# Optimization experiments

Hardware: AMD Instinct MI355X
Metric: run time of the kernel (lower is better)

The kernel has to match this reference:

```python
import jax, jax.numpy as jnp
import numpy as np

H = W = 32
C = 384
NH = 12
HEAD = C // NH
SCALE = HEAD ** -0.5
WS = 8            # window size
SS = 4            # shift size
N = WS * WS       # tokens per window (64)
NW = (H // WS) * (W // WS)  # windows per image (16)
HIDDEN = 4 * C
EPS = 1e-5
SQRT_2_OVER_PI = float(np.sqrt(2.0 / np.pi))


def _relative_position_index():
    ch = np.arange(WS)
    coords = np.stack(np.meshgrid(ch, ch, indexing='ij')).reshape(2, -1)  # [2, N]
    rel = (coords[:, :, None] - coords[:, None, :]).transpose(1, 2, 0)    # [N, N, 2]
    rel[:, :, 0] += WS - 1
    rel[:, :, 1] += WS - 1
    rel[:, :, 0] *= 2 * WS - 1
    return rel.sum(-1)  # [N, N] int


def _attn_mask():
    img = np.zeros((H, W), np.float32)
    sl = (slice(0, -WS), slice(-WS, -SS), slice(-SS, None))
    cnt = 0
    for hs in sl:
        for ws_ in sl:
            img[hs, ws_] = cnt
            cnt += 1
    m = img.reshape(H // WS, WS, W // WS, WS).transpose(0, 2, 1, 3).reshape(-1, N)  # [nW, N]
    am = m[:, None, :] - m[:, :, None]
    return np.where(am != 0, -100.0, 0.0).astype(np.float32)  # [nW, N, N]


REL_IDX = jnp.asarray(_relative_position_index())
ATTN_MASK = jnp.asarray(_attn_mask())


def _gelu(x):
    return x * 0.5 * (1.0 + jnp.tanh(SQRT_2_OVER_PI * (x + 0.044715 * x ** 3)))


def _layernorm(x, g, b):
    mu = jnp.mean(x, axis=-1, keepdims=True)
    var = jnp.mean(jnp.square(x - mu), axis=-1, keepdims=True)
    return (x - mu) * jax.lax.rsqrt(var + EPS) * g + b


def _window_partition(x):  # [B,H,W,C] -> [B*nW, N, C]
    B = x.shape[0]
    x = x.reshape(B, H // WS, WS, W // WS, WS, C).transpose(0, 1, 3, 2, 4, 5)
    return x.reshape(-1, N, C)


def _window_reverse(w, B):  # [B*nW, N, C] -> [B,H,W,C]
    x = w.reshape(B, H // WS, W // WS, WS, WS, C).transpose(0, 1, 3, 2, 4, 5)
    return x.reshape(B, H, W, C)


def setup_inputs() -> dict:
    key = jax.random.key(0)
    ks = jax.random.split(key, 16)
    s = 0.02
    return {
        'x': jax.random.normal(ks[0], (32, H * W, C), jnp.float32),
        'norm1_g': jnp.ones((C,), jnp.float32),
        'norm1_b': jnp.zeros((C,), jnp.float32),
        'qkv_w': jax.random.normal(ks[1], (C, 3 * C), jnp.float32) * s,
        'qkv_b': jnp.zeros((3 * C,), jnp.float32),
        'rel_bias_table': jax.random.normal(ks[2], ((2 * WS - 1) ** 2, NH), jnp.float32) * s,
        'proj_w': jax.random.normal(ks[3], (C, C), jnp.float32) * s,
        'proj_b': jnp.zeros((C,), jnp.float32),
        'norm2_g': jnp.ones((C,), jnp.float32),
        'norm2_b': jnp.zeros((C,), jnp.float32),
        'fc1_w': jax.random.normal(ks[4], (C, HIDDEN), jnp.float32) * s,
        'fc1_b': jnp.zeros((HIDDEN,), jnp.float32),
        'fc2_w': jax.random.normal(ks[5], (HIDDEN, C), jnp.float32) * s,
        'fc2_b': jnp.zeros((C,), jnp.float32),
    }


def reference(x, norm1_g, norm1_b, qkv_w, qkv_b, rel_bias_table, proj_w, proj_b,
              norm2_g, norm2_b, fc1_w, fc1_b, fc2_w, fc2_b):
    B = x.shape[0]
    shortcut = x
    y = _layernorm(x, norm1_g, norm1_b).reshape(B, H, W, C)
    y = jnp.roll(y, shift=(-SS, -SS), axis=(1, 2))          # cyclic shift
    win = _window_partition(y)                               # [B*nW, N, C]

    qkv = (win @ qkv_w + qkv_b).reshape(-1, N, 3, NH, HEAD).transpose(2, 0, 3, 1, 4)
    q, k, v = qkv[0], qkv[1], qkv[2]                         # [B*nW, NH, N, HEAD]
    attn = jnp.einsum('whnd,whmd->whnm', q * SCALE, k)       # [B*nW, NH, N, N]

    bias = rel_bias_table[REL_IDX.reshape(-1)].reshape(N, N, NH).transpose(2, 0, 1)
    attn = attn + bias[None]
    attn = attn.reshape(B, NW, NH, N, N) + ATTN_MASK[None, :, None]
    attn = jax.nn.softmax(attn.reshape(-1, NH, N, N), axis=-1)

    out = jnp.einsum('whnm,whmd->wnhd', attn, v).reshape(-1, N, C)
    out = out @ proj_w + proj_b                              # [B*nW, N, C]

    y = _window_reverse(out, B)
    y = jnp.roll(y, shift=(SS, SS), axis=(1, 2)).reshape(B, H * W, C)

    x = shortcut + y                                         # drop_path is identity (eval)
    h = _layernorm(x, norm2_g, norm2_b)
    h = _gelu(h @ fc1_w + fc1_b) @ fc2_w + fc2_b
    return x + h
```

## Files before the change

### kernel.cpp

```cpp
#include <hip/hip_runtime.h>
#include <hip/hip_bf16.h>
#include <math.h>

typedef __hip_bfloat16 bf16;
typedef __attribute__((ext_vector_type(8))) short short8;
typedef __attribute__((ext_vector_type(4))) float floatx4;

static constexpr int TOK = 32768;
static constexpr int CDIM = 384;
static constexpr int HID = 1536;

__device__ __forceinline__ bf16 f2bf(float v) { return __float2bfloat16(v); }

__device__ __forceinline__ unsigned short bf_bits(float a) {
  bf16 h = __float2bfloat16(a);
  unsigned short u;
  __builtin_memcpy(&u, &h, 2);
  return u;
}
__device__ __forceinline__ unsigned pack2(float a, float b) {
  return (unsigned)bf_bits(a) | ((unsigned)bf_bits(b) << 16);
}

typedef const __attribute__((address_space(1))) unsigned gas_t;
typedef __attribute__((address_space(3))) unsigned las_t;
__device__ __forceinline__ void gload16(const bf16* g, const bf16* l) {
  __builtin_amdgcn_global_load_lds((gas_t*)g, (las_t*)l, 16, 0, 0);
}

__global__ __launch_bounds__(256) void k_convt4(
    const float* __restrict__ s0, bf16* __restrict__ d0,
    const float* __restrict__ s1, bf16* __restrict__ d1,
    const float* __restrict__ s2, bf16* __restrict__ d2,
    const float* __restrict__ s3, bf16* __restrict__ d3) {
  int tid = blockIdx.x * 256 + threadIdx.x;
  const float* src; bf16* dst; int Kd, Nd, off;
  if (tid < 442368) { src = s0; dst = d0; Kd = 384; Nd = 1152; off = tid; }
  else if (tid < 589824) { src = s1; dst = d1; Kd = 384; Nd = 384; off = tid - 442368; }
  else if (tid < 1179648) { src = s2; dst = d2; Kd = 384; Nd = 1536; off = tid - 589824; }
  else { src = s3; dst = d3; Kd = 1536; Nd = 384; off = tid - 1179648; }
  int k = off / Nd, n = off - k * Nd;
  dst[(size_t)n * Kd + k] = f2bf(src[off]);
}

__global__ __launch_bounds__(256) void k_ln1(const float* __restrict__ x,
                                             const float* __restrict__ g,
                                             const float* __restrict__ b,
                                             bf16* __restrict__ out) {
  int wt = blockIdx.x * 4 + (threadIdx.x >> 6);
  int lane = threadIdx.x & 63;
  int win = wt >> 6, ntok = wt & 63;
  int bimg = win >> 4, wi = win & 15;
  int sh = (((wi >> 2) << 3) + (ntok >> 3) + 4) & 31;
  int sw = (((wi & 3) << 3) + (ntok & 7) + 4) & 31;
  const float* xr = x + ((size_t)bimg * 1024 + sh * 32 + sw) * CDIM;
  float v[6]; float s = 0.f, ss = 0.f;
#pragma unroll
  for (int j = 0; j < 6; ++j) {
    float t = xr[j * 64 + lane];
    v[j] = t; s += t; ss += t * t;
  }
#pragma unroll
  for (int off = 32; off > 0; off >>= 1) {
    s += __shfl_xor(s, off, 64);
    ss += __shfl_xor(ss, off, 64);
  }
  float mu = s * (1.f / 384.f);
  float var = ss * (1.f / 384.f) - mu * mu;
  float rs = rsqrtf(var + 1e-5f);
  bf16* orow = out + (size_t)wt * CDIM;
#pragma unroll
  for (int j = 0; j < 6; ++j) {
    int c = j * 64 + lane;
    orow[c] = f2bf((v[j] - mu) * rs * g[c] + b[c]);
  }
}

__global__ __launch_bounds__(256) void k_ln2(const float* __restrict__ x1,
                                             const float* __restrict__ g,
                                             const float* __restrict__ b,
                                             bf16* __restrict__ out) {
  int t = blockIdx.x * 4 + (threadIdx.x >> 6);
  int lane = threadIdx.x & 63;
  const float* xr = x1 + (size_t)t * CDIM;
  float v[6]; float s = 0.f, ss = 0.f;
#pragma unroll
  for (int j = 0; j < 6; ++j) {
    float q = xr[j * 64 + lane];
    v[j] = q; s += q; ss += q * q;
  }
#pragma unroll
  for (int off = 32; off > 0; off >>= 1) {
    s += __shfl_xor(s, off, 64);
    ss += __shfl_xor(ss, off, 64);
  }
  float mu = s * (1.f / 384.f);
  float var = ss * (1.f / 384.f) - mu * mu;
  float rs = rsqrtf(var + 1e-5f);
  bf16* orow = out + (size_t)t * CDIM;
#pragma unroll
  for (int j = 0; j < 6; ++j) {
    int c = j * 64 + lane;
    orow[c] = f2bf((v[j] - mu) * rs * g[c] + b[c]);
  }
}

template <int K, int EPI, int NT>
__global__ __launch_bounds__(256) void k_gemm(const bf16* __restrict__ A,
                                              const bf16* __restrict__ Bt,
                                              const float* __restrict__ bias,
                                              const float* __restrict__ extra,
                                              void* __restrict__ outp) {
  __shared__ __attribute__((aligned(16))) char pool[49152];
  bf16* A0 = (bf16*)pool;
  bf16* B0 = (bf16*)(pool + 8192);
  bf16* A1 = (bf16*)(pool + 16384);
  bf16* B1 = (bf16*)(pool + 24576);
  bf16* A2 = (bf16*)(pool + 32768);
  bf16* B2 = (bf16*)(pool + 40960);

  const int tid = threadIdx.x;
  const int wv = tid >> 6, lane = tid & 63;

  const int flat = blockIdx.x;
  const int xcd = flat & 7;
  const int idx = flat >> 3;
  const int rpx = (gridDim.x >> 3) / NT;
  const int cb = idx % NT;
  const int rb = idx / NT;
  const int mblk = (xcd * rpx + rb) * 128, nblk = cb * 128;

  const int srow = lane >> 3;
  const int sc = (lane & 7) ^ srow;
  const int srow2 = 2 * srow + (sc >> 2);
  const int gco = (sc & 3) * 8;
  const bf16* gaw = A + (size_t)(mblk + wv * 32 + srow2) * K + gco;
  const bf16* gbw = Bt + (size_t)(nblk + wv * 32 + srow2) * K + gco;
  bf16* lA0 = A0 + wv * 1024; bf16* lB0 = B0 + wv * 1024;
  bf16* lA1 = A1 + wv * 1024; bf16* lB1 = B1 + wv * 1024;
  bf16* lA2 = A2 + wv * 1024; bf16* lB2 = B2 + wv * 1024;

  const int wr = wv >> 1, wc = wv & 1;
  const int mr = lane & 15, q = lane >> 4;
  const int slot8 = ((((mr & 1) << 2) | q) ^ (mr >> 1)) * 8;
  const int faOff = (wr * 32 + (mr >> 1)) * 64 + slot8;
  const int fbOff = (wc * 32 + (mr >> 1)) * 64 + slot8;

  floatx4 acc[4][4];
#pragma unroll
  for (int i = 0; i < 4; ++i)
#pragma unroll
    for (int j = 0; j < 4; ++j) acc[i][j] = floatx4{0.f, 0.f, 0.f, 0.f};

#define VM4() asm volatile("s_waitcnt vmcnt(4)" ::: "memory")
#define VM0() asm volatile("s_waitcnt vmcnt(0)" ::: "memory")
#define BAR() __builtin_amdgcn_s_barrier()

#define STAGE(LA, LB, KOFF) do { \
    gload16(gaw + (KOFF), (LA)); \
    gload16(gaw + (KOFF) + 16 * K, (LA) + 512); \
    gload16(gbw + (KOFF), (LB)); \
    gload16(gbw + (KOFF) + 16 * K, (LB) + 512); \
  } while (0)

#define COMPUTE(ABASE, BBASE) do { \
    short8 a_[4], b_[4]; \
    _Pragma("unroll") \
    for (int mt = 0; mt < 4; ++mt) a_[mt] = *(const short8*)((ABASE) + faOff + mt * 512); \
    _Pragma("unroll") \
    for (int nt = 0; nt < 4; ++nt) b_[nt] = *(const short8*)((BBASE) + fbOff + nt * 512); \
    _Pragma("unroll") \
    for (int mt = 0; mt < 4; ++mt) \
      _Pragma("unroll") \
      for (int nt = 0; nt < 4; ++nt) \
        acc[mt][nt] = __builtin_amdgcn_mfma_f32_16x16x32_bf16(a_[mt], b_[nt], acc[mt][nt], 0, 0, 0); \
  } while (0)

  STAGE(lA0, lB0, 0);
  STAGE(lA1, lB1, 32);
  for (int k0 = 0; k0 < K - 96; k0 += 96) {
    VM4(); BAR(); STAGE(lA2, lB2, k0 + 64);  COMPUTE(A0, B0);
    VM4(); BAR(); STAGE(lA0, lB0, k0 + 96);  COMPUTE(A1, B1);
    VM4(); BAR(); STAGE(lA1, lB1, k0 + 128); COMPUTE(A2, B2);
  }
  VM4(); BAR(); STAGE(lA2, lB2, K - 32); COMPUTE(A0, B0);
  VM4(); BAR();                          COMPUTE(A1, B1);
  VM0(); BAR();                          COMPUTE(A2, B2);
#undef STAGE
#undef COMPUTE
#undef VM4
#undef VM0
#undef BAR

  __syncthreads();
  float* epsw = (float*)pool + wv * (16 * 68);
  const int rr = lane >> 2, c0 = (lane & 3) * 16;
#pragma unroll
  for (int mt = 0; mt < 4; ++mt) {
#pragma unroll
    for (int nt = 0; nt < 4; ++nt)
#pragma unroll
      for (int r = 0; r < 4; ++r)
        epsw[(q * 4 + r) * 68 + nt * 16 + mr] = acc[mt][nt][r];
    float v[16];
#pragma unroll
    for (int j = 0; j < 4; ++j) {
      float4 t = *(const float4*)&epsw[rr * 68 + c0 + j * 4];
      v[j * 4 + 0] = t.x; v[j * 4 + 1] = t.y; v[j * 4 + 2] = t.z; v[j * 4 + 3] = t.w;
    }
    const int grow = mblk + wr * 64 + mt * 16 + rr;
    const int gcol = nblk + wc * 64 + c0;

    if constexpr (EPI == 0) {
      int win = grow >> 6, ntok = grow & 63;
      int s = gcol / 384;
      int rem = gcol - s * 384;
      int h = rem >> 5, d0 = rem & 31;
      bf16* op = (bf16*)outp + (((size_t)s * 512 + win) * 12 + h) * 2048 + ntok * 32 + d0;
      uint4 pk;
      float bv[16];
#pragma unroll
      for (int j = 0; j < 16; ++j) bv[j] = v[j] + bias[gcol + j];
      pk.x = pack2(bv[0], bv[1]); pk.y = pack2(bv[2], bv[3]);
      pk.z = pack2(bv[4], bv[5]); pk.w = pack2(bv[6], bv[7]);
      *(uint4*)op = pk;
      pk.x = pack2(bv[8], bv[9]); pk.y = pack2(bv[10], bv[11]);
      pk.z = pack2(bv[12], bv[13]); pk.w = pack2(bv[14], bv[15]);
      *(uint4*)(op + 8) = pk;
    } else if constexpr (EPI == 1) {
      int win = grow >> 6, ntok = grow & 63;
      int bimg = win >> 4, wi = win & 15;
      int hh = (((wi >> 2) << 3) + (ntok >> 3) + 4) & 31;
      int ww = (((wi & 3) << 3) + (ntok & 7) + 4) & 31;
      size_t t = (size_t)bimg * 1024 + hh * 32 + ww;
      float* op = (float*)outp + t * CDIM + gcol;
      const float* xr = extra + t * CDIM + gcol;
#pragma unroll
      for (int j = 0; j < 4; ++j) {
        float4 xv = *(const float4*)(xr + j * 4);
        float4 ov;
        ov.x = xv.x + v[j * 4 + 0] + bias[gcol + j * 4 + 0];
        ov.y = xv.y + v[j * 4 + 1] + bias[gcol + j * 4 + 1];
        ov.z = xv.z + v[j * 4 + 2] + bias[gcol + j * 4 + 2];
        ov.w = xv.w + v[j * 4 + 3] + bias[gcol + j * 4 + 3];
        *(float4*)(op + j * 4) = ov;
      }
    }
  }
}

__global__ __launch_bounds__(512, 2) void k_mlp(const bf16* __restrict__ A,
                                                const bf16* __restrict__ W1t,
                                                const bf16* __restrict__ W2t,
                                                const float* __restrict__ b1,
                                                const float* __restrict__ b2,
                                                const float* __restrict__ x1,
                                                float* __restrict__ out) {
  __shared__ __attribute__((aligned(16))) char pool[131072];
  bf16* A0 = (bf16*)pool;
  bf16* A1 = (bf16*)(pool + 8192);
  bf16* A2 = (bf16*)(pool + 16384);
  bf16* W10 = (bf16*)(pool + 24576);
  bf16* W11 = (bf16*)(pool + 32768);
  bf16* W12 = (bf16*)(pool + 40960);
  bf16* hs = (bf16*)(pool + 49152);
  bf16* W2sA = (bf16*)(pool + 81920);
  bf16* W2sB = (bf16*)(pool + 106496);

  const int tid = threadIdx.x;
  const int wv = tid >> 6, lane = tid & 63;
  const int mblk = blockIdx.x * 128;

  const int srow = lane >> 3;
  const int sc = (lane & 7) ^ srow;
  const int srow2 = 2 * srow + (sc >> 2);
  const int gco = (sc & 3) * 8;

  const bf16* ga = A + (size_t)(mblk + wv * 16 + srow2) * 384 + gco;
  const bf16* g1 = W1t + (size_t)(wv * 16 + srow2) * 384 + gco;
  const bf16* g2 = W2t + (size_t)(wv * 48 + srow2) * 1536 + gco;

  const int wr1 = wv >> 2, wc1 = wv & 3;
  const int mr = lane & 15, q = lane >> 4;
  const int slot8 = ((((mr & 1) << 2) | q) ^ (mr >> 1)) * 8;
  const int faOff1 = (wr1 * 32 + (mr >> 1)) * 64 + slot8;
  const int fbOff1 = (wc1 * 16 + (mr >> 1)) * 64 + slot8;
  const int fbOff2 = (wc1 * 48 + (mr >> 1)) * 64 + slot8;
  const size_t hb = (size_t)(wr1 * 64 + mr) * 128;
  int px[4];
#pragma unroll
  for (int kk = 0; kk < 4; ++kk)
    px[kk] = (((kk & 2) << 2) | ((((kk & 1) << 2) | q) ^ (mr & 7))) * 8;

  floatx4 acc1[4][2];
  floatx4 acc2[4][6];
#pragma unroll
  for (int i = 0; i < 4; ++i) {
#pragma unroll
    for (int j = 0; j < 2; ++j) acc1[i][j] = floatx4{0.f, 0.f, 0.f, 0.f};
#pragma unroll
    for (int j = 0; j < 6; ++j) acc2[i][j] = floatx4{0.f, 0.f, 0.f, 0.f};
  }

#define VMW(N) asm volatile("s_waitcnt vmcnt(" #N ")" ::: "memory")
#define LGKM0() asm volatile("s_waitcnt lgkmcnt(0)" ::: "memory")
#define BARR() __builtin_amdgcn_s_barrier()
#define ST(ABUF, WBUF, G1P, KO) do { \
    gload16(ga + (KO), (ABUF) + wv * 512); \
    gload16((G1P) + (KO), (WBUF) + wv * 512); \
  } while (0)
#define STW2(BUF, KK, G2P) do { \
    _Pragma("unroll") \
    for (int g = 0; g < 3; ++g) \
      gload16((G2P) + (KK) * 32 + (size_t)g * 16 * 1536, (BUF) + wv * 1536 + g * 512); \
  } while (0)
#define C1(AB, WB) do { \
    short8 a_[4], b_[2]; \
    _Pragma("unroll") \
    for (int mt = 0; mt < 4; ++mt) a_[mt] = *(const short8*)((AB) + faOff1 + mt * 512); \
    b_[0] = *(const short8*)((WB) + fbOff1); \
    b_[1] = *(const short8*)((WB) + fbOff1 + 512); \
    _Pragma("unroll") \
    for (int mt = 0; mt < 4; ++mt) \
      _Pragma("unroll") \
      for (int nt = 0; nt < 2; ++nt) \
        acc1[mt][nt] = __builtin_amdgcn_mfma_f32_16x16x32_bf16(a_[mt], b_[nt], acc1[mt][nt], 0, 0, 0); \
  } while (0)
#define C2(BUF, KK) do { \
    short8 ha[4], wb[6]; \
    _Pragma("unroll") \
    for (int mt = 0; mt < 4; ++mt) \
      ha[mt] = *(const short8*)(hs + hb + mt * 2048 + px[KK]); \
    _Pragma("unroll") \
    for (int nt = 0; nt < 6; ++nt) \
      wb[nt] = *(const short8*)((BUF) + fbOff2 + nt * 512); \
    _Pragma("unroll") \
    for (int mt = 0; mt < 4; ++mt) \
      _Pragma("unroll") \
      for (int nt = 0; nt < 6; ++nt) \
        acc2[mt][nt] = __builtin_amdgcn_mfma_f32_16x16x32_bf16(ha[mt], wb[nt], acc2[mt][nt], 0, 0, 0); \
  } while (0)
#define GELU_H(BB0, BB1) do { \
    _Pragma("unroll") \
    for (int mt = 0; mt < 4; ++mt) { \
      const int tokb = wr1 * 64 + mt * 16 + q * 4; \
      _Pragma("unroll") \
      for (int nt = 0; nt < 2; ++nt) { \
        const float bb = nt ? (BB1) : (BB0); \
        const int sw = wc1 * 4 + nt * 2 + (mr >> 3); \
        const int s8 = sw & 8, s7 = sw & 7; \
        _Pragma("unroll") \
        for (int r = 0; r < 4; ++r) { \
          float z = acc1[mt][nt][r] + bb; \
          float t2 = z * z; \
          float cp = __builtin_fmaf(t2, -0.0713548162f, -1.5957691216f); \
          float e = __expf(z * cp); \
          float gl = z * __builtin_amdgcn_rcpf(1.f + e); \
          const int t7 = ((q & 1) << 2) | r; \
          hs[(size_t)(tokb + r) * 128 + (s8 | (s7 ^ t7)) * 8 + (mr & 7)] = f2bf(gl); \
        } \
        acc1[mt][nt] = floatx4{0.f, 0.f, 0.f, 0.f}; \
      } \
    } \
    LGKM0(); \
  } while (0)

  ST(A0, W10, g1, 0);
  ST(A1, W11, g1, 32);

  for (int ci = 0; ci < 12; ++ci) {
    BARR();
    const int cb = ci * 128;
    float bb0 = b1[cb + wc1 * 32 + mr];
    float bb1 = b1[cb + wc1 * 32 + 16 + mr];
    STW2(W2sA, 0, g2);
    STW2(W2sB, 1, g2);

    const bf16* g1n = g1 + 49152;
    VMW(8); BARR(); ST(A2, W12, g1, 64);   C1(A0, W10);
    VMW(8); BARR(); ST(A0, W10, g1, 96);   C1(A1, W11);
    VMW(2); BARR(); ST(A1, W11, g1, 128);  C1(A2, W12);
    VMW(2); BARR(); ST(A2, W12, g1, 160);  C1(A0, W10);
    VMW(2); BARR(); ST(A0, W10, g1, 192);  C1(A1, W11);
    VMW(2); BARR(); ST(A1, W11, g1, 224);  C1(A2, W12);
    VMW(2); BARR(); ST(A2, W12, g1, 256);  C1(A0, W10);
    VMW(2); BARR(); ST(A0, W10, g1, 288);  C1(A1, W11);
    VMW(2); BARR(); ST(A1, W11, g1, 320);  C1(A2, W12);
    VMW(2); BARR(); ST(A2, W12, g1, 352);  C1(A0, W10);
    VMW(2); BARR(); ST(A0, W10, g1n, 0);   C1(A1, W11);
    VMW(2); BARR(); ST(A1, W11, g1n, 32);  C1(A2, W12);

    GELU_H(bb0, bb1);
    __syncthreads();

    C2(W2sA, 0);
    BARR();
    STW2(W2sA, 2, g2);
    C2(W2sB, 1);
    BARR();
    STW2(W2sB, 3, g2);
    VMW(3); BARR();
    C2(W2sA, 2);
    VMW(0); BARR();
    C2(W2sB, 3);

    g1 += 49152;
    g2 += 128;
  }
#undef ST
#undef STW2
#undef C1
#undef C2
#undef GELU_H

  VMW(0);
  __syncthreads();

  float* epsw = (float*)(pool + wv * 6400);
  const int rr = lane >> 2, c4 = (lane & 3) * 24;
#pragma unroll
  for (int mt = 0; mt < 4; ++mt) {
#pragma unroll
    for (int nt = 0; nt < 6; ++nt)
#pragma unroll
      for (int r = 0; r < 4; ++r)
        epsw[(q * 4 + r) * 100 + nt * 16 + mr] = acc2[mt][nt][r];
    const int grow = mblk + wr1 * 64 + mt * 16 + rr;
    const int gcol = wc1 * 96 + c4;
    const float* xr = x1 + (size_t)grow * 384 + gcol;
    float* op = out + (size_t)grow * 384 + gcol;
#pragma unroll
    for (int j = 0; j < 6; ++j) {
      float4 t = *(const float4*)&epsw[rr * 100 + c4 + j * 4];
      float4 xv = *(const float4*)(xr + j * 4);
      float4 bv = *(const float4*)&b2[gcol + j * 4];
      float4 ov;
      ov.x = xv.x + t.x + bv.x;
      ov.y = xv.y + t.y + bv.y;
      ov.z = xv.z + t.z + bv.z;
      ov.w = xv.w + t.w + bv.w;
      *(float4*)(op + j * 4) = ov;
    }
  }
#undef VMW
#undef LGKM0
#undef BARR
}

__global__ __launch_bounds__(64) void k_attn(const bf16* __restrict__ qkv,
                                             const float* __restrict__ tblg,
                                             bf16* __restrict__ out) {
  __shared__ __attribute__((aligned(16))) char pool[16384];
  bf16* Qs = (bf16*)pool;
  bf16* Ks = (bf16*)(pool + 5120);
  bf16* Ps = (bf16*)pool;
  float* Os = (float*)pool;
  bf16* Vt = (bf16*)(pool + 10240);
  unsigned long long* msk = (unsigned long long*)(pool + 14848);
  float* tbl = (float*)(pool + 15360);

  const int bid = blockIdx.x;
  const int win = bid / 12, head = bid - win * 12;
  const int lane = threadIdx.x;
  const int q = lane >> 4, mr = lane & 15;

  for (int i = lane; i < 225; i += 64) tbl[i] = tblg[i * 12 + head];

  size_t base = ((size_t)win * 12 + head) * 2048 + lane * 32;
  const uint4* qp = (const uint4*)(qkv + base);
  const uint4* kp = (const uint4*)(qkv + (size_t)12582912 + base);
  const uint4* vp = (const uint4*)(qkv + (size_t)25165824 + base);
#pragma unroll
  for (int i = 0; i < 4; ++i) *(uint4*)(Qs + lane * 40 + i * 8) = qp[i];
#pragma unroll
  for (int i = 0; i < 4; ++i) *(uint4*)(Ks + lane * 40 + i * 8) = kp[i];
  {
    union { uint4 u[4]; unsigned short h[32]; } vv;
#pragma unroll
    for (int i = 0; i < 4; ++i) vv.u[i] = vp[i];
    unsigned short* VtU = (unsigned short*)Vt;
#pragma unroll
    for (int d = 0; d < 32; ++d) VtU[d * 72 + lane] = vv.h[d];
  }
  {
    int wi = win & 15;
    int ri = lane >> 3, ci = lane & 7;
    int rh = ((wi >> 2) << 3) + ri, rw = ((wi & 3) << 3) + ci;
    int rid = (rh < 24 ? 0 : (rh < 28 ? 1 : 2)) * 3 + (rw < 24 ? 0 : (rw < 28 ? 1 : 2));
    unsigned long long m = 0;
#pragma unroll
    for (int v = 0; v < 9; ++v) {
      unsigned long long bb = __ballot(rid == v);
      if (rid == v) m = bb;
    }
    msk[lane] = m;
  }

  floatx4 sac[4][4];
#pragma unroll
  for (int i = 0; i < 4; ++i)
#pragma unroll
    for (int j = 0; j < 4; ++j) sac[i][j] = floatx4{0.f, 0.f, 0.f, 0.f};
  {
    short8 af[4], bf[4];
#pragma unroll
    for (int t = 0; t < 4; ++t) af[t] = *(const short8*)(Qs + (t * 16 + mr) * 40 + q * 8);
#pragma unroll
    for (int t = 0; t < 4; ++t) bf[t] = *(const short8*)(Ks + (t * 16 + mr) * 40 + q * 8);
    __builtin_amdgcn_s_setprio(1);
#pragma unroll
    for (int mt = 0; mt < 4; ++mt)
#pragma unroll
      for (int nt = 0; nt < 4; ++nt)
        sac[mt][nt] = __builtin_amdgcn_mfma_f32_16x16x32_bf16(af[mt], bf[nt], sac[mt][nt], 0, 0, 0);
    __builtin_amdgcn_s_setprio(0);
  }

  float psum[4][4];
#pragma unroll
  for (int mt = 0; mt < 4; ++mt)
#pragma unroll
    for (int r = 0; r < 4; ++r) psum[mt][r] = 0.f;
#pragma unroll
  for (int mt = 0; mt < 4; ++mt) {
#pragma unroll
    for (int r = 0; r < 4; ++r) {
      const int i = mt * 16 + q * 4 + r;
      const unsigned long long mrow = msk[i];
      const int bi = (i >> 3) * 15 + (i & 7);
#pragma unroll
      for (int nt = 0; nt < 4; ++nt) {
        const int j = nt * 16 + mr;
        const int idx = bi + 112 - (j >> 3) * 15 - (j & 7);
        float val = sac[mt][nt][r] * 0.17677669529663687f + tbl[idx];
        float p = __expf(val);
        p = ((mrow >> j) & 1ull) ? p : 0.f;
        psum[mt][r] += p;
        Ps[i * 72 + j] = f2bf(p);
      }
    }
  }
  float inv[4][4];
#pragma unroll
  for (int mt = 0; mt < 4; ++mt)
#pragma unroll
    for (int r = 0; r < 4; ++r) {
      float s = psum[mt][r];
      s += __shfl_xor(s, 1, 64);
      s += __shfl_xor(s, 2, 64);
      s += __shfl_xor(s, 4, 64);
      s += __shfl_xor(s, 8, 64);
      inv[mt][r] = 1.f / s;
    }

  floatx4 oac[4][2];
#pragma unroll
  for (int i = 0; i < 4; ++i)
#pragma unroll
    for (int j = 0; j < 2; ++j) oac[i][j] = floatx4{0.f, 0.f, 0.f, 0.f};
#pragma unroll
  for (int kk = 0; kk < 2; ++kk) {
    short8 ap[4], bv[2];
#pragma unroll
    for (int mt = 0; mt < 4; ++mt)
      ap[mt] = *(const short8*)(Ps + (mt * 16 + mr) * 72 + kk * 32 + q * 8);
#pragma unroll
    for (int nt = 0; nt < 2; ++nt)
      bv[nt] = *(const short8*)(Vt + (nt * 16 + mr) * 72 + kk * 32 + q * 8);
    __builtin_amdgcn_s_setprio(1);
#pragma unroll
    for (int mt = 0; mt < 4; ++mt)
#pragma unroll
      for (int nt = 0; nt < 2; ++nt)
        oac[mt][nt] = __builtin_amdgcn_mfma_f32_16x16x32_bf16(ap[mt], bv[nt], oac[mt][nt], 0, 0, 0);
    __builtin_amdgcn_s_setprio(0);
  }

#pragma unroll
  for (int mt = 0; mt < 4; ++mt)
#pragma unroll
    for (int nt = 0; nt < 2; ++nt)
#pragma unroll
      for (int r = 0; r < 4; ++r)
        Os[(mt * 16 + q * 4 + r) * 40 + nt * 16 + mr] = oac[mt][nt][r] * inv[mt][r];
  float ov[32];
#pragma unroll
  for (int c = 0; c < 8; ++c) {
    const int cc = c ^ (lane & 7);
    float4 t = *(const float4*)(Os + lane * 40 + cc * 4);
    ov[cc * 4 + 0] = t.x; ov[cc * 4 + 1] = t.y;
    ov[cc * 4 + 2] = t.z; ov[cc * 4 + 3] = t.w;
  }
  uint4* o4 = (uint4*)(out + ((size_t)win * 64 + lane) * CDIM + head * 32);
#pragma unroll
  for (int i = 0; i < 4; ++i) {
    uint4 pk;
    pk.x = pack2(ov[i * 8 + 0], ov[i * 8 + 1]);
    pk.y = pack2(ov[i * 8 + 2], ov[i * 8 + 3]);
    pk.z = pack2(ov[i * 8 + 4], ov[i * 8 + 5]);
    pk.w = pack2(ov[i * 8 + 6], ov[i * 8 + 7]);
    o4[i] = pk;
  }
}

extern "C" void kernel_launch(void* const* d_in, const int* in_sizes, int n_in,
                              void* d_out, int out_size, void* d_ws, size_t ws_size,
                              hipStream_t stream) {
  const float* x = (const float*)d_in[0];
  const float* n1g = (const float*)d_in[1];
  const float* n1b = (const float*)d_in[2];
  const float* qkv_w = (const float*)d_in[3];
  const float* qkv_b = (const float*)d_in[4];
  const float* reltbl = (const float*)d_in[5];
  const float* proj_w = (const float*)d_in[6];
  const float* proj_b = (const float*)d_in[7];
  const float* n2g = (const float*)d_in[8];
  const float* n2b = (const float*)d_in[9];
  const float* fc1_w = (const float*)d_in[10];
  const float* fc1_b = (const float*)d_in[11];
  const float* fc2_w = (const float*)d_in[12];
  const float* fc2_b = (const float*)d_in[13];
  float* out = (float*)d_out;

  char* p = (char*)d_ws;
  bf16* w_qkv_t = (bf16*)p;  p += (size_t)442368 * 2;
  bf16* w_proj_t = (bf16*)p; p += (size_t)147456 * 2;
  bf16* w_fc1_t = (bf16*)p;  p += (size_t)589824 * 2;
  bf16* w_fc2_t = (bf16*)p;  p += (size_t)589824 * 2;
  bf16* bufA = (bf16*)p;     p += (size_t)12582912 * 2;
  bf16* qkvb = (bf16*)p;     p += (size_t)37748736 * 2;
  bf16* attno = (bf16*)p;    p += (size_t)12582912 * 2;
  float* x1 = (float*)p;     p += (size_t)12582912 * 4;

  k_convt4<<<dim3(6912), dim3(256), 0, stream>>>(qkv_w, w_qkv_t, proj_w, w_proj_t,
                                                 fc1_w, w_fc1_t, fc2_w, w_fc2_t);

  k_ln1<<<dim3(8192), dim3(256), 0, stream>>>(x, n1g, n1b, bufA);
  k_gemm<384, 0, 9><<<dim3(9 * 256), dim3(256), 0, stream>>>(bufA, w_qkv_t, qkv_b, nullptr, qkvb);
  k_attn<<<dim3(6144), dim3(64), 0, stream>>>(qkvb, reltbl, attno);
  k_gemm<384, 1, 3><<<dim3(3 * 256), dim3(256), 0, stream>>>(attno, w_proj_t, proj_b, x, x1);
  k_ln2<<<dim3(8192), dim3(256), 0, stream>>>(x1, n2g, n2b, bufA);
  k_mlp<<<dim3(256), dim3(512), 0, stream>>>(bufA, w_fc1_t, w_fc2_t, fc1_b, fc2_b, x1, out);
}
```

Measured before the change: 392.0 us.

## Read fc2 weight fragments straight from global and double-buffer fc1 with wider stages

The fused MLP kernel no longer stages W2 tiles in shared memory. Each wave now loads its fc2 B-operand fragments directly from global memory (expected to hit L2) inside the second GEMM. The fc1 loop drops from a triple-buffered k=32 pipeline to a double-buffered k=64 pipeline with full vmcnt waits, and shared memory shrinks from 128KB to 96KB. This removes LDS staging traffic and barriers for W2, but the global-load latency is no longer hidden by prefetch, and the fc1 loop has less load/compute overlap.

```diff
diff --git a/kernel.cpp b/kernel.cpp
--- a/kernel.cpp
+++ b/kernel.cpp
@@ -256,16 +256,12 @@
                                                 const float* __restrict__ b2,
                                                 const float* __restrict__ x1,
                                                 float* __restrict__ out) {
-  __shared__ __attribute__((aligned(16))) char pool[131072];
+  __shared__ __attribute__((aligned(16))) char pool[98304];
   bf16* A0 = (bf16*)pool;
-  bf16* A1 = (bf16*)(pool + 8192);
-  bf16* A2 = (bf16*)(pool + 16384);
-  bf16* W10 = (bf16*)(pool + 24576);
-  bf16* W11 = (bf16*)(pool + 32768);
-  bf16* W12 = (bf16*)(pool + 40960);
-  bf16* hs = (bf16*)(pool + 49152);
-  bf16* W2sA = (bf16*)(pool + 81920);
-  bf16* W2sB = (bf16*)(pool + 106496);
+  bf16* A1 = (bf16*)(pool + 16384);
+  bf16* W10 = (bf16*)(pool + 32768);
+  bf16* W11 = (bf16*)(pool + 49152);
+  bf16* hs = (bf16*)(pool + 65536);
 
   const int tid = threadIdx.x;
   const int wv = tid >> 6, lane = tid & 63;
@@ -278,15 +274,14 @@
 
   const bf16* ga = A + (size_t)(mblk + wv * 16 + srow2) * 384 + gco;
   const bf16* g1 = W1t + (size_t)(wv * 16 + srow2) * 384 + gco;
-  const bf16* g2 = W2t + (size_t)(wv * 48 + srow2) * 1536 + gco;
 
   const int wr1 = wv >> 2, wc1 = wv & 3;
   const int mr = lane & 15, q = lane >> 4;
   const int slot8 = ((((mr & 1) << 2) | q) ^ (mr >> 1)) * 8;
   const int faOff1 = (wr1 * 32 + (mr >> 1)) * 64 + slot8;
   const int fbOff1 = (wc1 * 16 + (mr >> 1)) * 64 + slot8;
-  const int fbOff2 = (wc1 * 48 + (mr >> 1)) * 64 + slot8;
   const size_t hb = (size_t)(wr1 * 64 + mr) * 128;
+  const bf16* gW2 = W2t + (size_t)(wc1 * 96 + mr) * 1536 + q * 8;
   int px[4];
 #pragma unroll
   for (int kk = 0; kk < 4; ++kk)
@@ -307,33 +302,34 @@
 #define BARR() __builtin_amdgcn_s_barrier()
 #define ST(ABUF, WBUF, G1P, KO) do { \
     gload16(ga + (KO), (ABUF) + wv * 512); \
+    gload16(ga + (KO) + 32, (ABUF) + 4096 + wv * 512); \
     gload16((G1P) + (KO), (WBUF) + wv * 512); \
+    gload16((G1P) + (KO) + 32, (WBUF) + 4096 + wv * 512); \
   } while (0)
-#define STW2(BUF, KK, G2P) do { \
-    _Pragma("unroll") \
-    for (int g = 0; g < 3; ++g) \
-      gload16((G2P) + (KK) * 32 + (size_t)g * 16 * 1536, (BUF) + wv * 1536 + g * 512); \
+#define C1X(AB, WB) do { \
+    _Pragma("unroll") \
+    for (int kk = 0; kk < 2; ++kk) { \
+      short8 a_[4], b_[2]; \
+      _Pragma("unroll") \
+      for (int mt = 0; mt < 4; ++mt) \
+        a_[mt] = *(const short8*)((AB) + kk * 4096 + faOff1 + mt * 512); \
+      b_[0] = *(const short8*)((WB) + kk * 4096 + fbOff1); \
+      b_[1] = *(const short8*)((WB) + kk * 4096 + fbOff1 + 512); \
+      _Pragma("unroll") \
+      for (int mt = 0; mt < 4; ++mt) \
+        _Pragma("unroll") \
+        for (int nt = 0; nt < 2; ++nt) \
+          acc1[mt][nt] = __builtin_amdgcn_mfma_f32_16x16x32_bf16(a_[mt], b_[nt], acc1[mt][nt], 0, 0, 0); \
+    } \
   } while (0)
-#define C1(AB, WB) do { \
-    short8 a_[4], b_[2]; \
-    _Pragma("unroll") \
-    for (int mt = 0; mt < 4; ++mt) a_[mt] = *(const short8*)((AB) + faOff1 + mt * 512); \
-    b_[0] = *(const short8*)((WB) + fbOff1); \
-    b_[1] = *(const short8*)((WB) + fbOff1 + 512); \
-    _Pragma("unroll") \
-    for (int mt = 0; mt < 4; ++mt) \
-      _Pragma("unroll") \
-      for (int nt = 0; nt < 2; ++nt) \
-        acc1[mt][nt] = __builtin_amdgcn_mfma_f32_16x16x32_bf16(a_[mt], b_[nt], acc1[mt][nt], 0, 0, 0); \
-  } while (0)
-#define C2(BUF, KK) do { \
+#define C2D(GW2C, KK) do { \
     short8 ha[4], wb[6]; \
     _Pragma("unroll") \
     for (int mt = 0; mt < 4; ++mt) \
       ha[mt] = *(const short8*)(hs + hb + mt * 2048 + px[KK]); \
     _Pragma("unroll") \
     for (int nt = 0; nt < 6; ++nt) \
-      wb[nt] = *(const short8*)((BUF) + fbOff2 + nt * 512); \
+      wb[nt] = *(const short8*)((GW2C) + (size_t)nt * 24576 + (KK) * 32); \
     _Pragma("unroll") \
     for (int mt = 0; mt < 4; ++mt) \
       _Pragma("unroll") \
@@ -366,51 +362,33 @@
   } while (0)
 
   ST(A0, W10, g1, 0);
-  ST(A1, W11, g1, 32);
 
   for (int ci = 0; ci < 12; ++ci) {
-    BARR();
-    const int cb = ci * 128;
-    float bb0 = b1[cb + wc1 * 32 + mr];
-    float bb1 = b1[cb + wc1 * 32 + 16 + mr];
-    STW2(W2sA, 0, g2);
-    STW2(W2sB, 1, g2);
-
+    float bb0 = b1[ci * 128 + wc1 * 32 + mr];
+    float bb1 = b1[ci * 128 + wc1 * 32 + 16 + mr];
     const bf16* g1n = g1 + 49152;
-    VMW(8); BARR(); ST(A2, W12, g1, 64);   C1(A0, W10);
-    VMW(8); BARR(); ST(A0, W10, g1, 96);   C1(A1, W11);
-    VMW(2); BARR(); ST(A1, W11, g1, 128);  C1(A2, W12);
-    VMW(2); BARR(); ST(A2, W12, g1, 160);  C1(A0, W10);
-    VMW(2); BARR(); ST(A0, W10, g1, 192);  C1(A1, W11);
-    VMW(2); BARR(); ST(A1, W11, g1, 224);  C1(A2, W12);
-    VMW(2); BARR(); ST(A2, W12, g1, 256);  C1(A0, W10);
-    VMW(2); BARR(); ST(A0, W10, g1, 288);  C1(A1, W11);
-    VMW(2); BARR(); ST(A1, W11, g1, 320);  C1(A2, W12);
-    VMW(2); BARR(); ST(A2, W12, g1, 352);  C1(A0, W10);
-    VMW(2); BARR(); ST(A0, W10, g1n, 0);   C1(A1, W11);
-    VMW(2); BARR(); ST(A1, W11, g1n, 32);  C1(A2, W12);
+    const bf16* gW2c = gW2 + ci * 128;
+
+    VMW(2); BARR(); ST(A1, W11, g1, 64);   C1X(A0, W10);
+    VMW(0); BARR(); ST(A0, W10, g1, 128);  C1X(A1, W11);
+    VMW(0); BARR(); ST(A1, W11, g1, 192);  C1X(A0, W10);
+    VMW(0); BARR(); ST(A0, W10, g1, 256);  C1X(A1, W11);
+    VMW(0); BARR(); ST(A1, W11, g1, 320);  C1X(A0, W10);
+    VMW(0); BARR(); ST(A0, W10, g1n, 0);   C1X(A1, W11);
 
     GELU_H(bb0, bb1);
     __syncthreads();
 
-    C2(W2sA, 0);
-    BARR();
-    STW2(W2sA, 2, g2);
-    C2(W2sB, 1);
-    BARR();
-    STW2(W2sB, 3, g2);
-    VMW(3); BARR();
-    C2(W2sA, 2);
-    VMW(0); BARR();
-    C2(W2sB, 3);
+    C2D(gW2c, 0);
+    C2D(gW2c, 1);
+    C2D(gW2c, 2);
+    C2D(gW2c, 3);
 
     g1 += 49152;
-    g2 += 128;
   }
 #undef ST
-#undef STW2
-#undef C1
-#undef C2
+#undef C1X
+#undef C2D
 #undef GELU_H
 
   VMW(0);
```

Result: slower. 435.0 us (+11.0%).
